# Optimization experiments

Hardware: AMD Instinct MI355X
Metric: run time of the kernel (lower is better)

The kernel has to match this reference:

```python
import jax, jax.numpy as jnp
import numpy as np

RHO = 1.0
EPSILON = 0.1
N_ITERS = 5
EPS = 1e-08


def setup_inputs() -> dict:
    key = jax.random.key(0)
    k1, k2, k3 = jax.random.split(key, 3)
    B, H, M, N, D = 16, 16, 256, 576, 1024
    # student cross-attention weights: positive, rows roughly sum to 1 (post-softmax in the real model)
    sa = jax.random.uniform(k1, (B, H, M, N), dtype=jnp.float32) + 1e-3
    student_attn = sa / sa.sum(axis=-1, keepdims=True)
    visual_feats = jax.random.normal(k2, (B, N, D), dtype=jnp.float32)
    text_feats = jax.random.normal(k3, (B, M, D), dtype=jnp.float32)
    text_mask = jnp.ones((B, M), dtype=jnp.float32)
    return {"student_attn": student_attn, "visual_feats": visual_feats,
            "text_feats": text_feats, "text_mask": text_mask}


def _l2norm(x):
    return x / jnp.sqrt(jnp.sum(x * x, axis=-1, keepdims=True) + 1e-12)


def _teacher_plan(x, y, y_mask):
    # x: (B,N,D) visual, y: (B,M,D) text, y_mask: (B,M)
    B, N, D = x.shape
    M = y.shape[1]
    x_n = _l2norm(x)
    y_n = _l2norm(y)
    cost = 1.0 - jnp.einsum('bmd,bnd->bmn', y_n, x_n)          # (B,M,N)
    mu = jnp.full((B, N, 1), 1.0 / N, dtype=x.dtype)            # visual marginal (column vec)
    nu = (y_mask / (jnp.sum(y_mask, axis=1, keepdims=True) + EPS))[:, :, None]  # (B,M,1)
    K = jnp.exp(-cost / EPSILON)                                # (B,M,N)
    fi = RHO / (RHO + EPSILON)
    u = jnp.ones((B, M, 1), dtype=x.dtype)
    v = jnp.ones((B, N, 1), dtype=x.dtype)
    for _ in range(N_ITERS):
        Kv = jnp.einsum('bmn,bnk->bmk', K, v)                   # (B,M,1)
        u = (nu / (Kv + EPS)) ** fi
        Ktu = jnp.einsum('bmn,bmk->bnk', K, u)                  # (B,N,1)
        v = (mu / (Ktu + EPS)) ** fi
    P = u * K * jnp.swapaxes(v, 1, 2)                           # (B,M,N)
    return P / (jnp.sum(P, axis=-1, keepdims=True) + EPS)


def reference(student_attn, visual_feats, text_feats, text_mask):
    teacher = jax.lax.stop_gradient(_teacher_plan(visual_feats, text_feats, text_mask))
    teacher = teacher[:, None, :, :]                            # (B,1,M,N)
    loss = -jnp.sum(teacher * jnp.log(student_attn + EPS), axis=-1)  # (B,H,M)
    loss = loss * text_mask[:, None, :]
    return jnp.mean(loss)
```

## Files before the change

### kernel.cpp

```cpp
#include <hip/hip_runtime.h>
#include <math.h>

#define B_ 16
#define H_ 16
#define M_ 256
#define N_ 576
#define D_ 1024
#define BK 64
#define LDS_STRIDE (BK + 8)
#define NROWS (B_ * N_ + B_ * M_)

constexpr float EPS_ = 1e-8f;
constexpr float FI_ = 0.90909090909090906f;

typedef __bf16 bf16x8 __attribute__((ext_vector_type(8)));
typedef float f32x4 __attribute__((ext_vector_type(4)));

__device__ __forceinline__ float wave_reduce(float v) {
#pragma unroll
  for (int o = 32; o > 0; o >>= 1) v += __shfl_down(v, o, 64);
  return v;
}

__device__ __forceinline__ unsigned short f2bf(float f) {
  union { float f; unsigned u; } a; a.f = f;
  unsigned r = a.u + 0x7fff + ((a.u >> 16) & 1);
  return (unsigned short)(r >> 16);
}

__device__ __forceinline__ float bits2f(unsigned u) {
  union { unsigned u; float f; } a; a.u = u;
  return a.f;
}

__global__ __launch_bounds__(256) void sumlog_kernel(const float* __restrict__ student,
                                                     float* __restrict__ SL) {
  const int b = blockIdx.y;
  const size_t mn4 = (size_t)blockIdx.x * 256 + threadIdx.x;
  const float* st = student + (size_t)b * H_ * M_ * N_ + mn4 * 4;
  float4 acc = {0.f, 0.f, 0.f, 0.f};
#pragma unroll
  for (int h = 0; h < H_; ++h) {
    float4 s4 = *(const float4*)&st[(size_t)h * M_ * N_];
    acc.x += __logf(s4.x + EPS_);
    acc.y += __logf(s4.y + EPS_);
    acc.z += __logf(s4.z + EPS_);
    acc.w += __logf(s4.w + EPS_);
  }
  *(float4*)&SL[(size_t)b * M_ * N_ + mn4 * 4] = acc;
}

__global__ __launch_bounds__(256) void prep_kernel(const float* __restrict__ vis,
                                                   const float* __restrict__ txt,
                                                   unsigned short* __restrict__ xb,
                                                   unsigned short* __restrict__ yb) {
  const int lane = threadIdx.x & 63;
  int wave = blockIdx.x * 4 + (threadIdx.x >> 6);
  const float* src;
  unsigned short* dst;
  if (wave < B_ * N_) {
    src = vis + (size_t)wave * D_;
    dst = xb + (size_t)wave * D_;
  } else {
    int r = wave - B_ * N_;
    src = txt + (size_t)r * D_;
    dst = yb + (size_t)r * D_;
  }
  float4 v[4];
  float s = 0.f;
#pragma unroll
  for (int it = 0; it < 4; ++it) {
    v[it] = *(const float4*)&src[it * 256 + lane * 4];
    s += v[it].x * v[it].x + v[it].y * v[it].y + v[it].z * v[it].z + v[it].w * v[it].w;
  }
  s = wave_reduce(s);
  s = __shfl(s, 0, 64);
  float inv = rsqrtf(s + 1e-12f);
#pragma unroll
  for (int it = 0; it < 4; ++it) {
    ushort4 pk;
    pk.x = f2bf(v[it].x * inv);
    pk.y = f2bf(v[it].y * inv);
    pk.z = f2bf(v[it].z * inv);
    pk.w = f2bf(v[it].w * inv);
    *(ushort4*)&dst[it * 256 + lane * 4] = pk;
  }
}

__global__ __launch_bounds__(256) void gemm_k_mfma(const unsigned short* __restrict__ xb,
                                                   const unsigned short* __restrict__ yb,
                                                   unsigned short* __restrict__ Kw) {
  __shared__ unsigned short As[64][LDS_STRIDE];
  __shared__ unsigned short Bs[64][LDS_STRIDE];
  const int b = blockIdx.z;
  const int m0 = blockIdx.y * 64;
  const int n0 = blockIdx.x * 64;
  const unsigned short* Y = yb + (size_t)b * M_ * D_;
  const unsigned short* X = xb + (size_t)b * N_ * D_;
  const int t = threadIdx.x;
  const int lane = t & 63;
  const int w = t >> 6;
  const int wm = (w & 1) * 32;
  const int wn = (w >> 1) * 32;
  const int lr = t >> 3;
  const int lc = (t & 7) * 8;
  const int fr = lane & 15;
  const int fk = (lane >> 4) * 8;

  f32x4 acc[2][2] = {};
  for (int k0 = 0; k0 < D_; k0 += BK) {
#pragma unroll
    for (int p = 0; p < 2; ++p) {
      *(uint4*)&As[lr + 32 * p][lc] = *(const uint4*)&Y[(size_t)(m0 + lr + 32 * p) * D_ + k0 + lc];
      *(uint4*)&Bs[lr + 32 * p][lc] = *(const uint4*)&X[(size_t)(n0 + lr + 32 * p) * D_ + k0 + lc];
    }
    __syncthreads();
#pragma unroll
    for (int ks = 0; ks < BK; ks += 32) {
      bf16x8 a[2], bfr[2];
#pragma unroll
      for (int i = 0; i < 2; ++i) {
        a[i] = *(const bf16x8*)&As[wm + i * 16 + fr][ks + fk];
        bfr[i] = *(const bf16x8*)&Bs[wn + i * 16 + fr][ks + fk];
      }
#pragma unroll
      for (int i = 0; i < 2; ++i)
#pragma unroll
        for (int j = 0; j < 2; ++j)
          acc[i][j] = __builtin_amdgcn_mfma_f32_16x16x32_bf16(a[i], bfr[j], acc[i][j], 0, 0, 0);
    }
    __syncthreads();
  }

  const int cm = (lane >> 4) * 4;
  const int cn = lane & 15;
#pragma unroll
  for (int i = 0; i < 2; ++i)
#pragma unroll
    for (int j = 0; j < 2; ++j)
#pragma unroll
      for (int rg = 0; rg < 4; ++rg) {
        int m = m0 + wm + i * 16 + cm + rg;
        int n = n0 + wn + j * 16 + cn;
        Kw[((size_t)b * M_ + m) * N_ + n] = f2bf(expf(10.f * (acc[i][j][rg] - 1.f)));
      }
}

__global__ __launch_bounds__(1024) void sinkloss_kernel(const unsigned short* __restrict__ Kw,
                                                        const float* __restrict__ SL,
                                                        const float* __restrict__ mask,
                                                        float* __restrict__ out) {
  __shared__ float partv[16][N_];
  __shared__ float sv[N_];
  __shared__ float su[M_];
  __shared__ float snu[M_];
  __shared__ float smask[M_];
  __shared__ float srow[M_];
  __shared__ float sred[16];
  const int b = blockIdx.x;
  const int t = threadIdx.x;
  const int lane = t & 63;
  const int w = t >> 6;
  const int r0 = w * 16;
  const unsigned short* Kb = Kw + (size_t)b * M_ * N_;

  float mv = (t < M_) ? mask[b * M_ + t] : 0.f;
  float wsum = wave_reduce(mv);
  if (t < M_ && lane == 0) sred[w] = wsum;
  if (t < N_) sv[t] = 1.f;
  if (t < M_) smask[t] = mv;
  __syncthreads();
  if (t < M_) {
    float msum = sred[0] + sred[1] + sred[2] + sred[3];
    snu[t] = mv / (msum + EPS_);
  }

  unsigned kreg[9][8];
#pragma unroll
  for (int j = 0; j < 9; ++j)
#pragma unroll
    for (int p = 0; p < 8; ++p) {
      unsigned lo = Kb[(size_t)(r0 + 2 * p) * N_ + lane + 64 * j];
      unsigned hi = Kb[(size_t)(r0 + 2 * p + 1) * N_ + lane + 64 * j];
      kreg[j][p] = lo | (hi << 16);
    }
#define KVAL(j, i) bits2f(((i) & 1) ? (kreg[j][(i) >> 1] & 0xffff0000u) : (kreg[j][(i) >> 1] << 16))

  __syncthreads();

  for (int it = 0; it < 5; ++it) {
#pragma unroll
    for (int i = 0; i < 16; ++i) {
      float s = 0.f;
#pragma unroll
      for (int j = 0; j < 9; ++j) s += KVAL(j, i) * sv[lane + 64 * j];
      s = wave_reduce(s);
      if (lane == 0) srow[r0 + i] = s;
    }
    __syncthreads();
    if (t < M_) su[t] = powf(snu[t] / (srow[t] + EPS_), FI_);
    __syncthreads();
#pragma unroll
    for (int j = 0; j < 9; ++j) {
      float s = 0.f;
#pragma unroll
      for (int i = 0; i < 16; ++i) s += KVAL(j, i) * su[r0 + i];
      partv[w][lane + 64 * j] = s;
    }
    __syncthreads();
    if (t < N_) {
      float s = 0.f;
#pragma unroll
      for (int ww = 0; ww < 16; ++ww) s += partv[ww][t];
      sv[t] = powf((1.f / (float)N_) / (s + EPS_), FI_);
    }
    __syncthreads();
  }

  float acc = 0.f;
#pragma unroll
  for (int i = 0; i < 16; ++i) {
    const int r = r0 + i;
    const float* slp = SL + ((size_t)b * M_ + r) * N_;
    float s1 = 0.f, s2 = 0.f;
#pragma unroll
    for (int j = 0; j < 9; ++j) {
      float kv = KVAL(j, i) * sv[lane + 64 * j];
      s1 += kv;
      s2 += kv * slp[lane + 64 * j];
    }
    s1 = wave_reduce(s1);
    s2 = wave_reduce(s2);
    if (lane == 0) acc -= smask[r] * s2 / (s1 + EPS_);
  }
  if (lane == 0) sred[w] = acc;
  __syncthreads();
  if (t == 0) {
    float tot = 0.f;
#pragma unroll
    for (int ww = 0; ww < 16; ++ww) tot += sred[ww];
    atomicAdd(out, tot * (1.f / ((float)B_ * H_ * M_)));
  }
#undef KVAL
}

extern "C" void kernel_launch(void* const* d_in, const int* in_sizes, int n_in,
                              void* d_out, int out_size, void* d_ws, size_t ws_size,
                              hipStream_t stream) {
  const float* student = (const float*)d_in[0];
  const float* vis = (const float*)d_in[1];
  const float* txt = (const float*)d_in[2];
  const float* mask = (const float*)d_in[3];
  float* out = (float*)d_out;

  char* p = (char*)d_ws;
  unsigned short* Kb = (unsigned short*)p; p += (size_t)B_ * M_ * N_ * 2;
  unsigned short* xb = (unsigned short*)p; p += (size_t)B_ * N_ * D_ * 2;
  unsigned short* yb = (unsigned short*)p; p += (size_t)B_ * M_ * D_ * 2;
  float* SL = (float*)p;      p += (size_t)B_ * M_ * N_ * 4;

  hipMemsetAsync(d_out, 0, sizeof(float), stream);
  sumlog_kernel<<<dim3(M_ * N_ / 4 / 256, B_), 256, 0, stream>>>(student, SL);
  prep_kernel<<<NROWS / 4, 256, 0, stream>>>(vis, txt, xb, yb);
  gemm_k_mfma<<<dim3(N_ / 64, M_ / 64, B_), 256, 0, stream>>>(xb, yb, Kb);
  sinkloss_kernel<<<B_, 1024, 0, stream>>>(Kb, SL, mask, out);
}
```

Before: 402.4 us.

## Split Sinkhorn loop into per-iteration multi-block kernels with deterministic final reduction

Replaces the single 16-block Sinkhorn+loss kernel with five per-iteration launches over a 9x16 grid. Each block redundantly recomputes the full Kv row sums and u, then produces one 64-column slice of v. The final loss is computed by a separate per-row kernel, and a single-block reduction replaces the atomicAdd and memset. This trades redundant Kv work and extra launches for far more blocks in flight than the 16 one-per-batch blocks before, though K is now re-read from global or L2 every iteration instead of being held in registers.

```diff
diff --git a/kernel.cpp b/kernel.cpp
--- a/kernel.cpp
+++ b/kernel.cpp
@@ -28,8 +28,8 @@
   return (unsigned short)(r >> 16);
 }
 
-__device__ __forceinline__ float bits2f(unsigned u) {
-  union { unsigned u; float f; } a; a.u = u;
+__device__ __forceinline__ float bf2f(unsigned short u) {
+  union { unsigned u; float f; } a; a.u = ((unsigned)u) << 16;
   return a.f;
 }
 
@@ -146,102 +146,95 @@
       }
 }
 
-__global__ __launch_bounds__(1024) void sinkloss_kernel(const unsigned short* __restrict__ Kw,
-                                                        const float* __restrict__ SL,
-                                                        const float* __restrict__ mask,
-                                                        float* __restrict__ out) {
-  __shared__ float partv[16][N_];
+__global__ __launch_bounds__(256) void sink_iter(const unsigned short* __restrict__ Kw,
+                                                 const float* __restrict__ mask,
+                                                 const float* __restrict__ vin,
+                                                 float* __restrict__ vout,
+                                                 int first) {
   __shared__ float sv[N_];
   __shared__ float su[M_];
-  __shared__ float snu[M_];
-  __shared__ float smask[M_];
-  __shared__ float srow[M_];
-  __shared__ float sred[16];
-  const int b = blockIdx.x;
+  __shared__ float part[4][64];
+  __shared__ float sred[4];
+  const int b = blockIdx.y;
+  const int j = blockIdx.x;
   const int t = threadIdx.x;
   const int lane = t & 63;
   const int w = t >> 6;
-  const int r0 = w * 16;
   const unsigned short* Kb = Kw + (size_t)b * M_ * N_;
 
-  float mv = (t < M_) ? mask[b * M_ + t] : 0.f;
-  float wsum = wave_reduce(mv);
-  if (t < M_ && lane == 0) sred[w] = wsum;
-  if (t < N_) sv[t] = 1.f;
-  if (t < M_) smask[t] = mv;
-  __syncthreads();
-  if (t < M_) {
-    float msum = sred[0] + sred[1] + sred[2] + sred[3];
-    snu[t] = mv / (msum + EPS_);
-  }
-
-  unsigned kreg[9][8];
-#pragma unroll
-  for (int j = 0; j < 9; ++j)
-#pragma unroll
-    for (int p = 0; p < 8; ++p) {
-      unsigned lo = Kb[(size_t)(r0 + 2 * p) * N_ + lane + 64 * j];
-      unsigned hi = Kb[(size_t)(r0 + 2 * p + 1) * N_ + lane + 64 * j];
-      kreg[j][p] = lo | (hi << 16);
-    }
-#define KVAL(j, i) bits2f(((i) & 1) ? (kreg[j][(i) >> 1] & 0xffff0000u) : (kreg[j][(i) >> 1] << 16))
-
-  __syncthreads();
-
-  for (int it = 0; it < 5; ++it) {
-#pragma unroll
-    for (int i = 0; i < 16; ++i) {
-      float s = 0.f;
-#pragma unroll
-      for (int j = 0; j < 9; ++j) s += KVAL(j, i) * sv[lane + 64 * j];
-      s = wave_reduce(s);
-      if (lane == 0) srow[r0 + i] = s;
-    }
-    __syncthreads();
-    if (t < M_) su[t] = powf(snu[t] / (srow[t] + EPS_), FI_);
-    __syncthreads();
-#pragma unroll
-    for (int j = 0; j < 9; ++j) {
-      float s = 0.f;
-#pragma unroll
-      for (int i = 0; i < 16; ++i) s += KVAL(j, i) * su[r0 + i];
-      partv[w][lane + 64 * j] = s;
-    }
-    __syncthreads();
-    if (t < N_) {
-      float s = 0.f;
-#pragma unroll
-      for (int ww = 0; ww < 16; ++ww) s += partv[ww][t];
-      sv[t] = powf((1.f / (float)N_) / (s + EPS_), FI_);
-    }
-    __syncthreads();
-  }
-
-  float acc = 0.f;
-#pragma unroll
-  for (int i = 0; i < 16; ++i) {
-    const int r = r0 + i;
-    const float* slp = SL + ((size_t)b * M_ + r) * N_;
-    float s1 = 0.f, s2 = 0.f;
-#pragma unroll
-    for (int j = 0; j < 9; ++j) {
-      float kv = KVAL(j, i) * sv[lane + 64 * j];
-      s1 += kv;
-      s2 += kv * slp[lane + 64 * j];
-    }
-    s1 = wave_reduce(s1);
-    s2 = wave_reduce(s2);
-    if (lane == 0) acc -= smask[r] * s2 / (s1 + EPS_);
-  }
-  if (lane == 0) sred[w] = acc;
-  __syncthreads();
-  if (t == 0) {
-    float tot = 0.f;
-#pragma unroll
-    for (int ww = 0; ww < 16; ++ww) tot += sred[ww];
-    atomicAdd(out, tot * (1.f / ((float)B_ * H_ * M_)));
-  }
-#undef KVAL
+  if (first) {
+    for (int i = t; i < N_; i += 256) sv[i] = 1.f;
+  } else {
+    for (int i = t; i < N_; i += 256) sv[i] = vin[b * N_ + i];
+  }
+  float mv = mask[b * M_ + t];
+  float ws = wave_reduce(mv);
+  if (lane == 0) sred[w] = ws;
+  __syncthreads();
+  const float msum = sred[0] + sred[1] + sred[2] + sred[3];
+
+  for (int i = 0; i < 64; ++i) {
+    const int m = w * 64 + i;
+    const unsigned short* rp = Kb + (size_t)m * N_;
+    float s = 0.f;
+#pragma unroll
+    for (int k = 0; k < 9; ++k) s += bf2f(rp[lane + 64 * k]) * sv[lane + 64 * k];
+    s = wave_reduce(s);
+    if (lane == 0) su[m] = s;
+  }
+  __syncthreads();
+  float uval = powf((mv / (msum + EPS_)) / (su[t] + EPS_), FI_);
+  __syncthreads();
+  su[t] = uval;
+  __syncthreads();
+
+  const int c = j * 64 + lane;
+  float s = 0.f;
+#pragma unroll 8
+  for (int m = w * 64; m < w * 64 + 64; ++m) s += bf2f(Kb[(size_t)m * N_ + c]) * su[m];
+  part[w][lane] = s;
+  __syncthreads();
+  if (t < 64) {
+    float tot = part[0][t] + part[1][t] + part[2][t] + part[3][t];
+    vout[b * N_ + j * 64 + t] = powf((1.f / (float)N_) / (tot + EPS_), FI_);
+  }
+}
+
+__global__ __launch_bounds__(256) void finloss_kernel(const unsigned short* __restrict__ Kw,
+                                                      const float* __restrict__ SL,
+                                                      const float* __restrict__ v,
+                                                      const float* __restrict__ mask,
+                                                      float* __restrict__ partial) {
+  const int b = blockIdx.y;
+  const int m = blockIdx.x * 4 + (threadIdx.x >> 6);
+  const int lane = threadIdx.x & 63;
+  const unsigned short* kp = Kw + ((size_t)b * M_ + m) * N_;
+  const float* slp = SL + ((size_t)b * M_ + m) * N_;
+  const float* vb = v + b * N_;
+  float s1 = 0.f, s2 = 0.f;
+#pragma unroll
+  for (int k = 0; k < 9; ++k) {
+    float kv = bf2f(kp[lane + 64 * k]) * vb[lane + 64 * k];
+    s1 += kv;
+    s2 += kv * slp[lane + 64 * k];
+  }
+  s1 = wave_reduce(s1);
+  s2 = wave_reduce(s2);
+  if (lane == 0) {
+    int row = b * M_ + m;
+    partial[row] = -mask[row] * s2 / ((s1 + EPS_) * (float)(B_ * H_ * M_));
+  }
+}
+
+__global__ __launch_bounds__(256) void reduce_kernel(const float* __restrict__ partial,
+                                                     float* __restrict__ out) {
+  __shared__ float red[4];
+  float s = 0.f;
+  for (int i = threadIdx.x; i < B_ * M_; i += 256) s += partial[i];
+  s = wave_reduce(s);
+  if ((threadIdx.x & 63) == 0) red[threadIdx.x >> 6] = s;
+  __syncthreads();
+  if (threadIdx.x == 0) out[0] = red[0] + red[1] + red[2] + red[3];
 }
 
 extern "C" void kernel_launch(void* const* d_in, const int* in_sizes, int n_in,
@@ -258,10 +251,20 @@
   unsigned short* xb = (unsigned short*)p; p += (size_t)B_ * N_ * D_ * 2;
   unsigned short* yb = (unsigned short*)p; p += (size_t)B_ * M_ * D_ * 2;
   float* SL = (float*)p;      p += (size_t)B_ * M_ * N_ * 4;
-
-  hipMemsetAsync(d_out, 0, sizeof(float), stream);
+  float* v0 = (float*)p;      p += B_ * N_ * 4;
+  float* v1 = (float*)p;      p += B_ * N_ * 4;
+  float* partial = (float*)p; p += B_ * M_ * 4;
+
   sumlog_kernel<<<dim3(M_ * N_ / 4 / 256, B_), 256, 0, stream>>>(student, SL);
   prep_kernel<<<NROWS / 4, 256, 0, stream>>>(vis, txt, xb, yb);
   gemm_k_mfma<<<dim3(N_ / 64, M_ / 64, B_), 256, 0, stream>>>(xb, yb, Kb);
-  sinkloss_kernel<<<B_, 1024, 0, stream>>>(Kb, SL, mask, out);
-}
+
+  sink_iter<<<dim3(9, B_), 256, 0, stream>>>(Kb, mask, v1, v0, 1);
+  sink_iter<<<dim3(9, B_), 256, 0, stream>>>(Kb, mask, v0, v1, 0);
+  sink_iter<<<dim3(9, B_), 256, 0, stream>>>(Kb, mask, v1, v0, 0);
+  sink_iter<<<dim3(9, B_), 256, 0, stream>>>(Kb, mask, v0, v1, 0);
+  sink_iter<<<dim3(9, B_), 256, 0, stream>>>(Kb, mask, v1, v0, 0);
+
+  finloss_kernel<<<dim3(M_ / 4, B_), 256, 0, stream>>>(Kb, SL, v0, mask, partial);
+  reduce_kernel<<<1, 256, 0, stream>>>(partial, out);
+}
```

Measured after the change: 496.3 us. +23.3%, slower.
